# Kernel tuning notes

Hardware: AMD Instinct MI355X
Metric: run time of the kernel (lower is better)

The kernel has to match this reference:

```python
import jax, jax.numpy as jnp
import numpy as np

N, E, D = 50000, 640000, 128
EPS = 1e-5

def _linear(x, w, b):
    return x @ w.T + b

def _batchnorm(x, gamma, beta):
    # torch_geometric BatchNorm (training mode): batch stats over row axis, biased var
    mu = jnp.mean(x, axis=0)
    var = jnp.mean((x - mu) ** 2, axis=0)
    return gamma * (x - mu) * jax.lax.rsqrt(var + EPS) + beta

def setup_inputs() -> dict:
    key = jax.random.key(0)
    ks = jax.random.split(key, 16)
    s = 0.05
    inp = {
        'h_in': jax.random.normal(ks[0], (N, D), jnp.float32),
        'e_in': jax.random.normal(ks[1], (E, D), jnp.float32),
        'edge_index': jax.random.randint(ks[2], (2, E), 0, N, jnp.int64),
    }
    for i, name in enumerate(['U', 'V', 'A', 'B', 'C']):
        inp[name + '_w'] = jax.random.normal(ks[3 + 2 * i], (D, D), jnp.float32) * s
        inp[name + '_b'] = jax.random.normal(ks[4 + 2 * i], (D,), jnp.float32) * s
    inp['h_gamma'] = jnp.ones((D,), jnp.float32)
    inp['h_beta'] = jnp.zeros((D,), jnp.float32)
    inp['e_gamma'] = jnp.ones((D,), jnp.float32)
    inp['e_beta'] = jnp.zeros((D,), jnp.float32)
    return inp

def reference(h_in, e_in, edge_index, U_w, U_b, V_w, V_b, A_w, A_b, B_w, B_b, C_w, C_b,
              h_gamma, h_beta, e_gamma, e_beta):
    dst, src = edge_index[0], edge_index[1]
    Uh = _linear(h_in, U_w, U_b)           # [N,D]
    Vh = _linear(h_in, V_w, V_b)           # [N,D]
    Ae = _linear(e_in, A_w, A_b)           # [E,D]
    Bh = _linear(h_in, B_w, B_b)           # [N,D]
    Ch = _linear(h_in, C_w, C_b)           # [N,D]
    sigmoid_e = jax.nn.sigmoid(e_in)       # edge_gates=True
    msgs = sigmoid_e * Vh[src]             # [E,D] gather + gate
    agg = jax.ops.segment_sum(msgs, dst, num_segments=N)  # global_add_pool
    h = h_in + jax.nn.relu(_batchnorm(Uh + agg, h_gamma, h_beta))
    e = e_in + jax.nn.relu(_batchnorm(Ae + Bh[dst] + Ch[src], e_gamma, e_beta))
    return (h, e)
```

## Files before the change

### kernel.cpp

```cpp
#include <hip/hip_runtime.h>
#include <hip/hip_bf16.h>
#include <math.h>

#define D 128
#define TILE 64
#define ESP 136

typedef __attribute__((ext_vector_type(8))) short s16x8;
typedef __attribute__((ext_vector_type(4))) float f32x4;

__device__ inline ushort f2bf(float x) {
    __hip_bfloat16 h = __float2bfloat16(x);
    return *reinterpret_cast<ushort*>(&h);
}
__device__ inline float bf16_to_f32(ushort h) {
    return __uint_as_float(((unsigned)h) << 16);
}

__device__ inline void cvt_hilo(f32x4 x0, f32x4 x1, s16x8& ah, s16x8& al) {
    #pragma unroll
    for (int j = 0; j < 4; ++j) {
        ushort hb = f2bf(x0[j]);
        ah[j] = (short)hb;
        al[j] = (short)f2bf(x0[j] - bf16_to_f32(hb));
        ushort hb2 = f2bf(x1[j]);
        ah[j + 4] = (short)hb2;
        al[j + 4] = (short)f2bf(x1[j] - bf16_to_f32(hb2));
    }
}

__global__ void zero_misc_k(float* stats, int* deg, int n) {
    int i = blockIdx.x * blockDim.x + threadIdx.x;
    if (i < 512) stats[i] = 0.f;
    if (i < n) deg[i] = 0;
}

__global__ void wconv5_k(const float* __restrict__ W0, const float* __restrict__ W1,
                         const float* __restrict__ W2, const float* __restrict__ W3,
                         const float* __restrict__ W4,
                         ushort* __restrict__ Fh, ushort* __restrict__ Fl) {
    int i = blockIdx.x * blockDim.x + threadIdx.x;
    if (i >= 5 * 16384) return;
    int wsel = i >> 14;
    int rem = i & 16383;
    int j = rem & 7;
    int l = (rem >> 3) & 63;
    int st = rem >> 9;
    int s = st >> 3, t = st & 7;
    int l15 = l & 15, lk = l >> 4;
    const float* W = wsel == 0 ? W0 : wsel == 1 ? W1 : wsel == 2 ? W2 : wsel == 3 ? W3 : W4;
    float x = W[(size_t)(t * 16 + l15) * D + s * 32 + lk * 8 + j];
    ushort h = f2bf(x);
    Fh[i] = h;
    Fl[i] = f2bf(x - bf16_to_f32(h));
}

__global__ __launch_bounds__(256, 4)
void node_linear_k(const float* __restrict__ h_in,
                   const ushort* __restrict__ Fh, const ushort* __restrict__ Fl,
                   const float* __restrict__ Ub, const float* __restrict__ Vb,
                   const float* __restrict__ Bb, const float* __restrict__ Cb,
                   float* __restrict__ outU, ushort* __restrict__ outV,
                   ushort* __restrict__ outB, ushort* __restrict__ outC,
                   int M)
{
    const int tid = threadIdx.x;
    const int w = tid >> 6, l = tid & 63;
    const int l15 = l & 15, lk = l >> 4;
    const int row0 = blockIdx.x * TILE;

    s16x8 ahs[4], als[4];
    {
        int arow = row0 + w * 16 + l15;
        if (arow >= M) arow = M - 1;
        const float* hr = h_in + (size_t)arow * D;
        #pragma unroll
        for (int s = 0; s < 4; ++s) {
            f32x4 x0 = *reinterpret_cast<const f32x4*>(hr + s * 32 + lk * 8);
            f32x4 x1 = *reinterpret_cast<const f32x4*>(hr + s * 32 + lk * 8 + 4);
            cvt_hilo(x0, x1, ahs[s], als[s]);
        }
    }

    const int mrow0 = row0 + w * 16 + lk * 4;

    #pragma unroll
    for (int wsel = 0; wsel < 4; ++wsel) {
        f32x4 acc[8];
        #pragma unroll
        for (int n = 0; n < 8; ++n) acc[n] = (f32x4){0.f, 0.f, 0.f, 0.f};

        #pragma unroll
        for (int s = 0; s < 4; ++s) {
            #pragma unroll
            for (int t = 0; t < 8; ++t) {
                size_t fo = ((size_t)((wsel * 32 + s * 8 + t) * 64 + l)) * 8;
                s16x8 bh = *reinterpret_cast<const s16x8*>(Fh + fo);
                s16x8 bl = *reinterpret_cast<const s16x8*>(Fl + fo);
                acc[t] = __builtin_amdgcn_mfma_f32_16x16x32_bf16(ahs[s], bh, acc[t], 0, 0, 0);
                acc[t] = __builtin_amdgcn_mfma_f32_16x16x32_bf16(ahs[s], bl, acc[t], 0, 0, 0);
                acc[t] = __builtin_amdgcn_mfma_f32_16x16x32_bf16(als[s], bh, acc[t], 0, 0, 0);
                if ((t & 1) == 1 && t < 7) __builtin_amdgcn_sched_barrier(0);
            }
        }

        const float* bias = wsel == 0 ? Ub : wsel == 1 ? Vb : wsel == 2 ? Bb : Cb;
        float bv[8];
        #pragma unroll
        for (int n = 0; n < 8; ++n) bv[n] = bias[n * 16 + l15];
        #pragma unroll
        for (int r = 0; r < 4; ++r) {
            int row = mrow0 + r;
            if (row < M) {
                if (wsel == 0) {
                    float* orow = outU + (size_t)row * D;
                    #pragma unroll
                    for (int n = 0; n < 8; ++n)
                        orow[n * 16 + l15] = acc[n][r] + bv[n];
                } else {
                    ushort* orow = (wsel == 1 ? outV : wsel == 2 ? outB : outC) + (size_t)row * D;
                    #pragma unroll
                    for (int n = 0; n < 8; ++n)
                        orow[n * 16 + l15] = f2bf(acc[n][r] + bv[n]);
                }
            }
        }
    }
}

__global__ void hist_k(const int* __restrict__ dst, int* __restrict__ deg, int E) {
    for (int e = blockIdx.x * blockDim.x + threadIdx.x; e < E; e += gridDim.x * blockDim.x)
        atomicAdd(&deg[dst[e]], 1);
}

__global__ void scan_k(const int* __restrict__ deg, int* __restrict__ off,
                       int* __restrict__ cursor, int n)
{
    __shared__ int wsum[16], wpre[16];
    const int tid = threadIdx.x, lane = tid & 63, w = tid >> 6;
    int carry = 0;
    for (int base = 0; base < n; base += 1024) {
        int i = base + tid;
        int v = (i < n) ? deg[i] : 0;
        int x = v;
        #pragma unroll
        for (int d = 1; d < 64; d <<= 1) {
            int t = __shfl_up(x, d);
            if (lane >= d) x += t;
        }
        if (lane == 63) wsum[w] = x;
        __syncthreads();
        if (tid == 0) {
            int run = carry;
            #pragma unroll
            for (int j = 0; j < 16; ++j) { int t = wsum[j]; wpre[j] = run; run += t; }
            carry = run;
        }
        __syncthreads();
        int excl = wpre[w] + x - v;
        if (i < n) { off[i] = excl; cursor[i] = excl; }
    }
    if (tid == 0) off[n] = carry;
}

__global__ void scatter_k(const int* __restrict__ dst, int* __restrict__ cursor,
                          int* __restrict__ perm, int E)
{
    for (int e = blockIdx.x * blockDim.x + threadIdx.x; e < E; e += gridDim.x * blockDim.x) {
        int pos = atomicAdd(&cursor[dst[e]], 1);
        perm[pos] = e;
    }
}

__global__ __launch_bounds__(256, 5)
void edge_k(const float* __restrict__ e_in,
            const int* __restrict__ eidx,
            const int* __restrict__ perm,
            const ushort* __restrict__ AFh, const ushort* __restrict__ AFl,
            const float* __restrict__ Ab,
            const ushort* __restrict__ Vh, const ushort* __restrict__ Bh,
            const ushort* __restrict__ Ch,
            float* __restrict__ out_h, float* __restrict__ out_e,
            float* __restrict__ e_sum, float* __restrict__ e_sq,
            int E)
{
    __shared__ int eids[TILE], dns[TILE], sns[TILE];
    __shared__ ushort es[TILE * ESP];
    __shared__ float sbuf[512], qbuf[512];

    const int tid = threadIdx.x;
    const int w = tid >> 6;
    const int l = tid & 63;
    const int l15 = l & 15;
    const int lk = l >> 4;
    const int e0 = blockIdx.x * TILE;

    if (tid < TILE) {
        int e = e0 + tid;
        int ec = e < E ? e : E - 1;
        int eid = perm[ec];
        eids[tid] = eid;
        dns[tid] = eidx[eid];
        sns[tid] = eidx[(size_t)E + eid];
    }
    __syncthreads();

    f32x4 acc[8];
    #pragma unroll
    for (int n = 0; n < 8; ++n) acc[n] = (f32x4){0.f, 0.f, 0.f, 0.f};

    {
        const int arow = w * 16 + l15;
        const float* er = e_in + (size_t)eids[arow] * D;
        f32x4 x0 = __builtin_nontemporal_load(
            reinterpret_cast<const f32x4*>(er + lk * 8));
        f32x4 x1 = __builtin_nontemporal_load(
            reinterpret_cast<const f32x4*>(er + lk * 8 + 4));
        #pragma unroll
        for (int s = 0; s < 4; ++s) {
            f32x4 n0, n1;
            if (s < 3) {
                n0 = __builtin_nontemporal_load(
                    reinterpret_cast<const f32x4*>(er + (s + 1) * 32 + lk * 8));
                n1 = __builtin_nontemporal_load(
                    reinterpret_cast<const f32x4*>(er + (s + 1) * 32 + lk * 8 + 4));
            }
            s16x8 ah, al;
            cvt_hilo(x0, x1, ah, al);
            *reinterpret_cast<s16x8*>(&es[arow * ESP + s * 32 + lk * 8]) = ah;
            #pragma unroll
            for (int t = 0; t < 8; ++t) {
                size_t fo = ((size_t)((s * 8 + t) * 64 + l)) * 8;
                s16x8 bh = *reinterpret_cast<const s16x8*>(AFh + fo);
                s16x8 bl = *reinterpret_cast<const s16x8*>(AFl + fo);
                acc[t] = __builtin_amdgcn_mfma_f32_16x16x32_bf16(ah, bh, acc[t], 0, 0, 0);
                acc[t] = __builtin_amdgcn_mfma_f32_16x16x32_bf16(ah, bl, acc[t], 0, 0, 0);
                acc[t] = __builtin_amdgcn_mfma_f32_16x16x32_bf16(al, bh, acc[t], 0, 0, 0);
                if ((t & 1) == 1 && t < 7) __builtin_amdgcn_sched_barrier(0);
            }
            if (s < 3) { x0 = n0; x1 = n1; }
        }
    }

    const int mrow0 = w * 16 + lk * 4;
    #pragma unroll
    for (int h = 0; h < 2; ++h) {
        float abv[4], sst[4], sq[4], rs[4];
        #pragma unroll
        for (int n = 0; n < 4; ++n) {
            abv[n] = Ab[(h * 4 + n) * 16 + l15];
            sst[n] = 0.f; sq[n] = 0.f; rs[n] = 0.f;
        }
        #pragma unroll
        for (int r = 0; r < 4; ++r) {
            int row = mrow0 + r;
            int eid = eids[row], dn = dns[row], sn = sns[row];
            bool valid = (e0 + row) < E;
            if (valid) {
                const ushort* br = Bh + (size_t)dn * D;
                const ushort* cr = Ch + (size_t)sn * D;
                float* oe = out_e + (size_t)eid * D;
                #pragma unroll
                for (int n = 0; n < 4; ++n) {
                    int col = (h * 4 + n) * 16 + l15;
                    float pre = acc[h * 4 + n][r] + abv[n]
                              + bf16_to_f32(br[col]) + bf16_to_f32(cr[col]);
                    __builtin_nontemporal_store(pre, oe + col);
                    sst[n] += pre;
                    sq[n] += pre * pre;
                }
            }
            const ushort* vr = Vh + (size_t)sn * D;
            #pragma unroll
            for (int n = 0; n < 4; ++n) {
                int col = (h * 4 + n) * 16 + l15;
                float ein = bf16_to_f32(es[row * ESP + col]);
                float m = valid ? bf16_to_f32(vr[col]) / (1.f + __expf(-ein)) : 0.f;
                rs[n] += m;
            }
            bool flush = (r == 3) || (dns[row + 1] != dn);
            if (flush) {
                float* dst = out_h + (size_t)dn * D;
                #pragma unroll
                for (int n = 0; n < 4; ++n) {
                    unsafeAtomicAdd(dst + (h * 4 + n) * 16 + l15, rs[n]);
                    rs[n] = 0.f;
                }
            }
            if (r & 1) __builtin_amdgcn_sched_barrier(0);
        }
        #pragma unroll
        for (int n = 0; n < 4; ++n) {
            sst[n] += __shfl_xor(sst[n], 16); sst[n] += __shfl_xor(sst[n], 32);
            sq[n]  += __shfl_xor(sq[n], 16);  sq[n]  += __shfl_xor(sq[n], 32);
        }
        if (l < 16) {
            #pragma unroll
            for (int n = 0; n < 4; ++n) {
                sbuf[w * 128 + (h * 4 + n) * 16 + l] = sst[n];
                qbuf[w * 128 + (h * 4 + n) * 16 + l] = sq[n];
            }
        }
    }
    __syncthreads();
    if (tid < 128) {
        float ss = sbuf[tid] + sbuf[128 + tid] + sbuf[256 + tid] + sbuf[384 + tid];
        float qq = qbuf[tid] + qbuf[128 + tid] + qbuf[256 + tid] + qbuf[384 + tid];
        unsafeAtomicAdd(&e_sum[tid], ss);
        unsafeAtomicAdd(&e_sq[tid], qq);
    }
}

__global__ void col_stats_k(const float* __restrict__ X, int rows,
                            float* __restrict__ sum, float* __restrict__ sumsq)
{
    __shared__ float sr[8][128], qr[8][128];
    const int tx = threadIdx.x & 31;
    const int rp = threadIdx.x >> 5;
    float4 s = make_float4(0.f, 0.f, 0.f, 0.f);
    float4 q = make_float4(0.f, 0.f, 0.f, 0.f);
    for (int r = blockIdx.x * 8 + rp; r < rows; r += gridDim.x * 8) {
        float4 v = *reinterpret_cast<const float4*>(X + (size_t)r * D + 4 * tx);
        s.x += v.x; q.x += v.x * v.x;
        s.y += v.y; q.y += v.y * v.y;
        s.z += v.z; q.z += v.z * v.z;
        s.w += v.w; q.w += v.w * v.w;
    }
    *reinterpret_cast<float4*>(&sr[rp][4 * tx]) = s;
    *reinterpret_cast<float4*>(&qr[rp][4 * tx]) = q;
    __syncthreads();
    if (threadIdx.x < 128) {
        float ss = 0.f, qq = 0.f;
        #pragma unroll
        for (int t = 0; t < 8; ++t) { ss += sr[t][threadIdx.x]; qq += qr[t][threadIdx.x]; }
        unsafeAtomicAdd(&sum[threadIdx.x], ss);
        unsafeAtomicAdd(&sumsq[threadIdx.x], qq);
    }
}

__global__ void finalize_k(const float* __restrict__ res_in,
                           float* __restrict__ out,
                           const float* __restrict__ sum, const float* __restrict__ sumsq,
                           const float* __restrict__ gamma, const float* __restrict__ beta,
                           float cntInv, int rows)
{
    const int tx = threadIdx.x & 31;
    const int rp = threadIdx.x >> 5;
    const int col4 = 4 * tx;
    float mu[4], g[4], b[4];
    #pragma unroll
    for (int i = 0; i < 4; ++i) {
        float m = sum[col4 + i] * cntInv;
        float var = sumsq[col4 + i] * cntInv - m * m;
        mu[i] = m;
        g[i] = gamma[col4 + i] * rsqrtf(var + 1e-5f);
        b[i] = beta[col4 + i];
    }
    for (int r = blockIdx.x * 8 + rp; r < rows; r += gridDim.x * 8) {
        size_t o = (size_t)r * D + col4;
        float4 x = *reinterpret_cast<const float4*>(out + o);
        float4 rr = *reinterpret_cast<const float4*>(res_in + o);
        float4 y;
        y.x = rr.x + fmaxf(g[0] * (x.x - mu[0]) + b[0], 0.f);
        y.y = rr.y + fmaxf(g[1] * (x.y - mu[1]) + b[1], 0.f);
        y.z = rr.z + fmaxf(g[2] * (x.z - mu[2]) + b[2], 0.f);
        y.w = rr.w + fmaxf(g[3] * (x.w - mu[3]) + b[3], 0.f);
        *reinterpret_cast<float4*>(out + o) = y;
    }
}

extern "C" void kernel_launch(void* const* d_in, const int* in_sizes, int n_in,
                              void* d_out, int out_size, void* d_ws, size_t ws_size,
                              hipStream_t stream)
{
    const float* h_in = (const float*)d_in[0];
    const float* e_in = (const float*)d_in[1];
    const int*   eidx = (const int*)d_in[2];
    const float* Uw = (const float*)d_in[3];  const float* Ub = (const float*)d_in[4];
    const float* Vw = (const float*)d_in[5];  const float* Vb = (const float*)d_in[6];
    const float* Aw = (const float*)d_in[7];  const float* Ab = (const float*)d_in[8];
    const float* Bw = (const float*)d_in[9];  const float* Bb = (const float*)d_in[10];
    const float* Cw = (const float*)d_in[11]; const float* Cb = (const float*)d_in[12];
    const float* hg = (const float*)d_in[13]; const float* hb = (const float*)d_in[14];
    const float* eg = (const float*)d_in[15]; const float* eb = (const float*)d_in[16];

    const int N = in_sizes[0] / D;
    const int E = in_sizes[1] / D;

    float* out_h = (float*)d_out;
    float* out_e = out_h + (size_t)N * D;

    ushort* Vh16 = (ushort*)d_ws;
    ushort* Bh16 = Vh16 + (size_t)N * D;
    ushort* Ch16 = Bh16 + (size_t)N * D;
    float* stats = (float*)(Ch16 + (size_t)N * D);
    float* h_sum = stats;       float* h_sq = stats + 128;
    float* e_sum = stats + 256; float* e_sq = stats + 384;
    int* deg    = (int*)(stats + 512);
    int* off    = deg + N;
    int* cursor = off + N + 1;
    int* perm   = cursor + N;
    ushort* Fh = (ushort*)(perm + E);
    ushort* Fl = Fh + 5 * 16384;

    zero_misc_k<<<(N + 255) / 256, 256, 0, stream>>>(stats, deg, N);
    wconv5_k<<<(5 * 16384 + 255) / 256, 256, 0, stream>>>(Uw, Vw, Bw, Cw, Aw, Fh, Fl);
    hist_k<<<1024, 256, 0, stream>>>(eidx, deg, E);
    scan_k<<<1, 1024, 0, stream>>>(deg, off, cursor, N);
    scatter_k<<<1024, 256, 0, stream>>>(eidx, cursor, perm, E);
    node_linear_k<<<(N + TILE - 1) / TILE, 256, 0, stream>>>(
        h_in, Fh, Fl, Ub, Vb, Bb, Cb, out_h, Vh16, Bh16, Ch16, N);
    edge_k<<<(E + TILE - 1) / TILE, 256, 0, stream>>>(
        e_in, eidx, perm, Fh + 4 * 16384, Fl + 4 * 16384, Ab, Vh16, Bh16, Ch16,
        out_h, out_e, e_sum, e_sq, E);
    col_stats_k<<<256, 256, 0, stream>>>(out_h, N, h_sum, h_sq);
    finalize_k<<<256, 256, 0, stream>>>(h_in, out_h, h_sum, h_sq, hg, hb, 1.0f / (float)N, N);
    finalize_k<<<2048, 256, 0, stream>>>(e_in, out_e, e_sum, e_sq, eg, eb, 1.0f / (float)E, E);
}
```

Baseline: 865.5 us.

## Store bf16 node features in lane-interleaved layout for vectorized edge gathers

The node-linear kernel now writes the V, B and C bf16 rows in a permuted column order, so each lane's 8 columns sit next to each other and go out as one 16-byte store. The edge kernel then gathers those rows with a single 16-byte load per lane instead of many 2-byte scalar loads. It also merges the two half-passes into one loop and writes the pre-norm edge values as two vector stores in the same permuted order. A new finalize kernel undoes the permutation with strided reads within each row, which adds some uncoalesced access in the final pass and more live registers in the edge kernel.

Result: no change. 856.7 us (-1.0%).

```diff
diff --git a/kernel.cpp b/kernel.cpp
--- a/kernel.cpp
+++ b/kernel.cpp
@@ -119,9 +119,11 @@
                         orow[n * 16 + l15] = acc[n][r] + bv[n];
                 } else {
                     ushort* orow = (wsel == 1 ? outV : wsel == 2 ? outB : outC) + (size_t)row * D;
+                    s16x8 pk;
                     #pragma unroll
                     for (int n = 0; n < 8; ++n)
-                        orow[n * 16 + l15] = f2bf(acc[n][r] + bv[n]);
+                        pk[n] = (short)f2bf(acc[n][r] + bv[n]);
+                    *reinterpret_cast<s16x8*>(orow + l15 * 8) = pk;
                 }
             }
         }
@@ -180,7 +182,7 @@
             const float* __restrict__ Ab,
             const ushort* __restrict__ Vh, const ushort* __restrict__ Bh,
             const ushort* __restrict__ Ch,
-            float* __restrict__ out_h, float* __restrict__ out_e,
+            float* __restrict__ out_h, float* __restrict__ out_pre,
             float* __restrict__ e_sum, float* __restrict__ e_sq,
             int E)
 {
@@ -242,64 +244,69 @@
         }
     }
 
+    float abv[8];
+    #pragma unroll
+    for (int n = 0; n < 8; ++n) abv[n] = Ab[n * 16 + l15];
+
+    float sst[8], sq[8], rs[8];
+    #pragma unroll
+    for (int n = 0; n < 8; ++n) { sst[n] = 0.f; sq[n] = 0.f; rs[n] = 0.f; }
+
     const int mrow0 = w * 16 + lk * 4;
     #pragma unroll
-    for (int h = 0; h < 2; ++h) {
-        float abv[4], sst[4], sq[4], rs[4];
-        #pragma unroll
-        for (int n = 0; n < 4; ++n) {
-            abv[n] = Ab[(h * 4 + n) * 16 + l15];
-            sst[n] = 0.f; sq[n] = 0.f; rs[n] = 0.f;
-        }
-        #pragma unroll
-        for (int r = 0; r < 4; ++r) {
-            int row = mrow0 + r;
-            int eid = eids[row], dn = dns[row], sn = sns[row];
-            bool valid = (e0 + row) < E;
-            if (valid) {
-                const ushort* br = Bh + (size_t)dn * D;
-                const ushort* cr = Ch + (size_t)sn * D;
-                float* oe = out_e + (size_t)eid * D;
-                #pragma unroll
-                for (int n = 0; n < 4; ++n) {
-                    int col = (h * 4 + n) * 16 + l15;
-                    float pre = acc[h * 4 + n][r] + abv[n]
-                              + bf16_to_f32(br[col]) + bf16_to_f32(cr[col]);
-                    __builtin_nontemporal_store(pre, oe + col);
-                    sst[n] += pre;
-                    sq[n] += pre * pre;
-                }
-            }
-            const ushort* vr = Vh + (size_t)sn * D;
+    for (int r = 0; r < 4; ++r) {
+        int row = mrow0 + r;
+        int eid = eids[row], dn = dns[row], sn = sns[row];
+        bool valid = (e0 + row) < E;
+        s16x8 br8 = *reinterpret_cast<const s16x8*>(Bh + (size_t)dn * D + l15 * 8);
+        s16x8 cr8 = *reinterpret_cast<const s16x8*>(Ch + (size_t)sn * D + l15 * 8);
+        s16x8 vr8 = *reinterpret_cast<const s16x8*>(Vh + (size_t)sn * D + l15 * 8);
+        if (valid) {
+            f32x4 p0, p1;
             #pragma unroll
             for (int n = 0; n < 4; ++n) {
-                int col = (h * 4 + n) * 16 + l15;
-                float ein = bf16_to_f32(es[row * ESP + col]);
-                float m = valid ? bf16_to_f32(vr[col]) / (1.f + __expf(-ein)) : 0.f;
-                rs[n] += m;
-            }
-            bool flush = (r == 3) || (dns[row + 1] != dn);
-            if (flush) {
-                float* dst = out_h + (size_t)dn * D;
-                #pragma unroll
-                for (int n = 0; n < 4; ++n) {
-                    unsafeAtomicAdd(dst + (h * 4 + n) * 16 + l15, rs[n]);
-                    rs[n] = 0.f;
-                }
-            }
-            if (r & 1) __builtin_amdgcn_sched_barrier(0);
-        }
-        #pragma unroll
-        for (int n = 0; n < 4; ++n) {
-            sst[n] += __shfl_xor(sst[n], 16); sst[n] += __shfl_xor(sst[n], 32);
-            sq[n]  += __shfl_xor(sq[n], 16);  sq[n]  += __shfl_xor(sq[n], 32);
-        }
-        if (l < 16) {
+                p0[n] = acc[n][r] + abv[n]
+                      + bf16_to_f32((ushort)br8[n]) + bf16_to_f32((ushort)cr8[n]);
+                p1[n] = acc[n + 4][r] + abv[n + 4]
+                      + bf16_to_f32((ushort)br8[n + 4]) + bf16_to_f32((ushort)cr8[n + 4]);
+            }
+            float* op = out_pre + (size_t)eid * D + l15 * 8;
+            __builtin_nontemporal_store(p0, reinterpret_cast<f32x4*>(op));
+            __builtin_nontemporal_store(p1, reinterpret_cast<f32x4*>(op + 4));
             #pragma unroll
             for (int n = 0; n < 4; ++n) {
-                sbuf[w * 128 + (h * 4 + n) * 16 + l] = sst[n];
-                qbuf[w * 128 + (h * 4 + n) * 16 + l] = sq[n];
-            }
+                sst[n] += p0[n];     sq[n] += p0[n] * p0[n];
+                sst[n + 4] += p1[n]; sq[n + 4] += p1[n] * p1[n];
+            }
+        }
+        #pragma unroll
+        for (int n = 0; n < 8; ++n) {
+            float ein = bf16_to_f32(es[row * ESP + n * 16 + l15]);
+            float m = valid ? bf16_to_f32((ushort)vr8[n]) / (1.f + __expf(-ein)) : 0.f;
+            rs[n] += m;
+        }
+        bool flush = (r == 3) || (dns[row + 1] != dn);
+        if (flush) {
+            float* dst = out_h + (size_t)dn * D;
+            #pragma unroll
+            for (int n = 0; n < 8; ++n) {
+                unsafeAtomicAdd(dst + n * 16 + l15, rs[n]);
+                rs[n] = 0.f;
+            }
+        }
+        if (r & 1) __builtin_amdgcn_sched_barrier(0);
+    }
+
+    #pragma unroll
+    for (int n = 0; n < 8; ++n) {
+        sst[n] += __shfl_xor(sst[n], 16); sst[n] += __shfl_xor(sst[n], 32);
+        sq[n]  += __shfl_xor(sq[n], 16);  sq[n]  += __shfl_xor(sq[n], 32);
+    }
+    if (l < 16) {
+        #pragma unroll
+        for (int n = 0; n < 8; ++n) {
+            sbuf[w * 128 + n * 16 + l] = sst[n];
+            qbuf[w * 128 + n * 16 + l] = sq[n];
         }
     }
     __syncthreads();
@@ -366,6 +373,42 @@
         y.z = rr.z + fmaxf(g[2] * (x.z - mu[2]) + b[2], 0.f);
         y.w = rr.w + fmaxf(g[3] * (x.w - mu[3]) + b[3], 0.f);
         *reinterpret_cast<float4*>(out + o) = y;
+    }
+}
+
+__global__ void finalize_perm_k(const float* __restrict__ res_in,
+                                float* out,
+                                const float* __restrict__ sum, const float* __restrict__ sumsq,
+                                const float* __restrict__ gamma, const float* __restrict__ beta,
+                                float cntInv, int rows)
+{
+    const int tx = threadIdx.x & 31;
+    const int rp = threadIdx.x >> 5;
+    const int col4 = 4 * tx;
+    float mu[4], g[4], b[4];
+    #pragma unroll
+    for (int i = 0; i < 4; ++i) {
+        float m = sum[col4 + i] * cntInv;
+        float var = sumsq[col4 + i] * cntInv - m * m;
+        mu[i] = m;
+        g[i] = gamma[col4 + i] * rsqrtf(var + 1e-5f);
+        b[i] = beta[col4 + i];
+    }
+    for (int r = blockIdx.x * 8 + rp; r < rows; r += gridDim.x * 8) {
+        size_t base = (size_t)r * D;
+        float x[4];
+        #pragma unroll
+        for (int i = 0; i < 4; ++i) {
+            int j = col4 + i;
+            x[i] = out[base + (j & 15) * 8 + (j >> 4)];
+        }
+        float4 rr = *reinterpret_cast<const float4*>(res_in + base + col4);
+        float4 y;
+        y.x = rr.x + fmaxf(g[0] * (x[0] - mu[0]) + b[0], 0.f);
+        y.y = rr.y + fmaxf(g[1] * (x[1] - mu[1]) + b[1], 0.f);
+        y.z = rr.z + fmaxf(g[2] * (x[2] - mu[2]) + b[2], 0.f);
+        y.w = rr.w + fmaxf(g[3] * (x[3] - mu[3]) + b[3], 0.f);
+        *reinterpret_cast<float4*>(out + base + col4) = y;
     }
 }
 
@@ -415,5 +458,5 @@
         out_h, out_e, e_sum, e_sq, E);
     col_stats_k<<<256, 256, 0, stream>>>(out_h, N, h_sum, h_sq);
     finalize_k<<<256, 256, 0, stream>>>(h_in, out_h, h_sum, h_sq, hg, hb, 1.0f / (float)N, N);
-    finalize_k<<<2048, 256, 0, stream>>>(e_in, out_e, e_sum, e_sq, eg, eb, 1.0f / (float)E, E);
-}
+    finalize_perm_k<<<2048, 256, 0, stream>>>(e_in, out_e, e_sum, e_sq, eg, eb, 1.0f / (float)E, E);
+}
```
